# Kernel optimization log

Measured on AMD Instinct MI355X. Metric: run time of the kernel, lower is better.

The kernel has to match this reference:

```python
import jax, jax.numpy as jnp
import numpy as np

B, N, D = 256, 64, 256   # graphs, nodes/graph, hidden dim (node_size*extend_dim)
T, E = B * N, 524288     # total nodes, total edges
NODE, BOND, K = 128, 16, 3
RRELU_SLOPE = (1.0 / 8.0 + 1.0 / 3.0) / 2.0  # eval-mode RReLU slope


def rrelu(x):
    return jnp.where(x >= 0, x, RRELU_SLOPE * x)


def conv_step(x, src, dst, ea, Wn, We, bm, Ws, bs):
    # message on each edge, scatter-add to destination, self-transform + update
    msg = jax.nn.relu(x[src] @ Wn + ea @ We + bm)          # [E, D]
    agg = jax.ops.segment_sum(msg, dst, num_segments=T)    # [T, D]
    return jax.nn.relu(x @ Ws + agg + bs)


def readout(x):
    # GlobalPool: cat([mean, sum, sort_pool(k=3)], -1) -> [B, 5D]
    xr = x.reshape(B, N, D)
    mean, s = xr.mean(1), xr.sum(1)
    order = jnp.argsort(-xr[..., -1], axis=1)[:, :K]                      # [B, K]
    topk = jnp.take_along_axis(xr, order[..., None], axis=1).reshape(B, K * D)
    return jnp.concatenate([mean, s, topk], -1)


def dot_pool(x1, x2):
    # per-graph cross-molecule dot product, max & mean -> [B, 2]
    item = jnp.einsum('bnd,bmd->bnm', x1.reshape(B, N, D), x2.reshape(B, N, D))
    return jnp.stack([item.max((1, 2)), item.mean((1, 2))], -1)


def setup_inputs() -> dict:
    key = jax.random.key(0)
    ks = jax.random.split(key, 32)
    batch = jnp.repeat(jnp.arange(B, dtype=jnp.int64), N)
    off = jnp.repeat(jnp.arange(B, dtype=jnp.int64) * N, E // B)

    def edges(k):
        s = jax.random.randint(k, (2, E), 0, N).astype(jnp.int64) + off[None, :]
        return s

    def w(k, shape):
        fan = shape[0]
        return jax.random.normal(k, shape, jnp.float32) * (1.0 / np.sqrt(fan))

    return {
        'x1': jax.random.normal(ks[0], (T, NODE), jnp.float32),
        'edge_index1': edges(ks[1]),
        'edge_attr1': jax.random.normal(ks[2], (E, BOND), jnp.float32),
        'batch1': batch,
        'x2': jax.random.normal(ks[3], (T, NODE), jnp.float32),
        'edge_index2': edges(ks[4]),
        'edge_attr2': jax.random.normal(ks[5], (E, BOND), jnp.float32),
        'batch2': batch,
        'W0_1': w(ks[6], (NODE, D)), 'b0_1': jnp.zeros(D),
        'W0_2': w(ks[7], (NODE, D)), 'b0_2': jnp.zeros(D),
        'Wn1': w(ks[8], (D, D)), 'We1': w(ks[9], (BOND, D)), 'bm1': jnp.zeros(D),
        'Ws1': w(ks[10], (D, D)), 'bs1': jnp.zeros(D),
        'Wn2': w(ks[11], (D, D)), 'We2': w(ks[12], (BOND, D)), 'bm2': jnp.zeros(D),
        'Ws2': w(ks[13], (D, D)), 'bs2': jnp.zeros(D),
        'Wf1': w(ks[14], (5 * D, D)), 'bf1': jnp.zeros(D),
        'Wf2': w(ks[15], (5 * D, D)), 'bf2': jnp.zeros(D),
        'Wo1': w(ks[16], (2 * D + 6, D)), 'bo1': jnp.zeros(D),
        'Wo2': w(ks[17], (D, 2)), 'bo2': jnp.zeros(2),
    }


def reference(x1, edge_index1, edge_attr1, batch1, x2, edge_index2, edge_attr2, batch2,
              W0_1, b0_1, W0_2, b0_2,
              Wn1, We1, bm1, Ws1, bs1,
              Wn2, We2, bm2, Ws2, bs2,
              Wf1, bf1, Wf2, bf2, Wo1, bo1, Wo2, bo2):
    xm1 = rrelu(x1 @ W0_1 + b0_1)
    xm2 = rrelu(x2 @ W0_2 + b0_2)
    s1, d1 = edge_index1[0], edge_index1[1]
    s2, d2 = edge_index2[0], edge_index2[1]
    fusion = []
    for _ in range(3):  # message_steps
        xm1 = conv_step(xm1, s1, d1, edge_attr1, Wn1, We1, bm1, Ws1, bs1)
        xm2 = conv_step(xm2, s2, d2, edge_attr2, Wn2, We2, bm2, Ws2, bs2)
        fusion.append(dot_pool(xm1, xm2))
    outm1 = readout(xm1) @ Wf1 + bf1
    outm2 = readout(xm2) @ Wf2 + bf2
    out = jnp.concatenate([outm1, outm2, jnp.concatenate(fusion, -1)], -1)
    out = out @ Wo1 + bo1
    return out @ Wo2 + bo2
```

## Files before the change

### kernel.cpp

```cpp
#include <hip/hip_runtime.h>
#include <hip/hip_fp16.h>

#define E_TOTAL 524288
#define RRELU_SLOPE 0.22916666666666666f
#define NKSPLIT 10

typedef float f32x4 __attribute__((ext_vector_type(4)));
typedef short short8_t __attribute__((ext_vector_type(8)));
typedef _Float16 half4_t __attribute__((ext_vector_type(4)));
typedef _Float16 h2v __attribute__((ext_vector_type(2)));

#define MFMA16F16 __builtin_amdgcn_mfma_f32_16x16x16f16

#if defined(__HIP_DEVICE_COMPILE__)
# if __has_builtin(__builtin_amdgcn_cvt_pkrtz)
#  define HAVE_PKRTZ 1
# endif
#endif

__device__ inline unsigned short f2bf(float x) {
  unsigned int u = __float_as_uint(x);
  u += 0x7FFFu + ((u >> 16) & 1u);
  return (unsigned short)(u >> 16);
}

__device__ inline unsigned int pack_h2(float a, float b) {
  __half2 h = __floats2half2_rn(a, b);
  return __builtin_bit_cast(unsigned int, h);
}

__device__ inline unsigned int pack_h2_fast(float a, float b) {
#ifdef HAVE_PKRTZ
  return __builtin_bit_cast(unsigned int, __builtin_amdgcn_cvt_pkrtz(a, b));
#else
  return pack_h2(a, b);
#endif
}

__global__ __launch_bounds__(256) void gemm_bf16_dual(
    const float* __restrict__ A1, const unsigned short* __restrict__ BT1,
    const float* __restrict__ bias1, float* __restrict__ C1,
    unsigned short* __restrict__ Ch1,
    const float* __restrict__ A2, const unsigned short* __restrict__ BT2,
    const float* __restrict__ bias2, float* __restrict__ C2,
    unsigned short* __restrict__ Ch2,
    int lda, int ldc, int K, int act)
{
  const float* A = blockIdx.z ? A2 : A1;
  const unsigned short* BT = blockIdx.z ? BT2 : BT1;
  const float* bias = blockIdx.z ? bias2 : bias1;
  float* C = blockIdx.z ? C2 : C1;
  unsigned short* Ch = blockIdx.z ? Ch2 : Ch1;

  __shared__ unsigned short As[128][32];
  __shared__ unsigned short Bs[128][32];
  const int tid = threadIdx.x;
  const int bm = blockIdx.x, bn = blockIdx.y;
  const int w = tid >> 6, l = tid & 63;
  const int wm = (w & 1) * 64, wn = (w >> 1) * 64;
  const int q = l >> 4, r = l & 15;

  f32x4 acc[4][4];
  for (int i = 0; i < 4; ++i)
    for (int j = 0; j < 4; ++j)
      acc[i][j] = (f32x4){0.f, 0.f, 0.f, 0.f};

  const int sm = tid >> 1;
  const int sk = (tid & 1) * 16;
  const float* ap = A + (size_t)(bm * 128 + sm) * lda + sk;
  const unsigned short* bp = BT + (size_t)(bn * 128 + sm) * K + sk;

  for (int k0 = 0; k0 < K; k0 += 32) {
    float4 f0 = *(const float4*)(ap + k0);
    float4 f1 = *(const float4*)(ap + k0 + 4);
    float4 f2 = *(const float4*)(ap + k0 + 8);
    float4 f3 = *(const float4*)(ap + k0 + 12);
    uint4 p0, p1;
    p0.x = (unsigned)f2bf(f0.x) | ((unsigned)f2bf(f0.y) << 16);
    p0.y = (unsigned)f2bf(f0.z) | ((unsigned)f2bf(f0.w) << 16);
    p0.z = (unsigned)f2bf(f1.x) | ((unsigned)f2bf(f1.y) << 16);
    p0.w = (unsigned)f2bf(f1.z) | ((unsigned)f2bf(f1.w) << 16);
    p1.x = (unsigned)f2bf(f2.x) | ((unsigned)f2bf(f2.y) << 16);
    p1.y = (unsigned)f2bf(f2.z) | ((unsigned)f2bf(f2.w) << 16);
    p1.z = (unsigned)f2bf(f3.x) | ((unsigned)f2bf(f3.y) << 16);
    p1.w = (unsigned)f2bf(f3.z) | ((unsigned)f2bf(f3.w) << 16);
    *(uint4*)&As[sm][sk] = p0;
    *(uint4*)&As[sm][sk + 8] = p1;
    uint4 b0 = *(const uint4*)(bp + k0);
    uint4 b1 = *(const uint4*)(bp + k0 + 8);
    *(uint4*)&Bs[sm][sk] = b0;
    *(uint4*)&Bs[sm][sk + 8] = b1;
    __syncthreads();

    short8_t af[4], bfr[4];
    for (int mt = 0; mt < 4; ++mt)
      af[mt] = *(const short8_t*)&As[wm + mt * 16 + r][q * 8];
    for (int nt = 0; nt < 4; ++nt)
      bfr[nt] = *(const short8_t*)&Bs[wn + nt * 16 + r][q * 8];
    for (int mt = 0; mt < 4; ++mt)
      for (int nt = 0; nt < 4; ++nt)
        acc[mt][nt] = __builtin_amdgcn_mfma_f32_16x16x32_bf16(
            af[mt], bfr[nt], acc[mt][nt], 0, 0, 0);
    __syncthreads();
  }

  for (int nt = 0; nt < 4; ++nt) {
    int gc = bn * 128 + wn + nt * 16 + r;
    float bv = bias ? bias[gc] : 0.f;
    for (int mt = 0; mt < 4; ++mt) {
      int gm = bm * 128 + wm + mt * 16 + q * 4;
      for (int rr = 0; rr < 4; ++rr) {
        float v = acc[mt][nt][rr] + bv;
        if (act == 2) v = (v >= 0.f) ? v : v * RRELU_SLOPE;
        if (Ch) Ch[(size_t)(gm + rr) * ldc + gc] = f2bf(v);
        else    C[(size_t)(gm + rr) * ldc + gc] = v;
      }
    }
  }
}

__global__ __launch_bounds__(256) void gemm_h_dual(
    const unsigned short* __restrict__ Ah1, const unsigned short* __restrict__ BT1,
    const float* __restrict__ bias1, unsigned int* __restrict__ yp1,
    float* __restrict__ y2o1,
    const unsigned short* __restrict__ Ah2, const unsigned short* __restrict__ BT2,
    const float* __restrict__ bias2, unsigned int* __restrict__ yp2,
    float* __restrict__ y2o2,
    int K)
{
  const unsigned short* A = blockIdx.z ? Ah2 : Ah1;
  const unsigned short* BT = blockIdx.z ? BT2 : BT1;
  const float* bias = blockIdx.z ? bias2 : bias1;
  unsigned int* yp = blockIdx.z ? yp2 : yp1;
  float* y2o = blockIdx.z ? y2o2 : y2o1;

  __shared__ unsigned short As[128][32];
  __shared__ unsigned short Bs[128][32];
  const int tid = threadIdx.x;
  const int bm = blockIdx.x, bn = blockIdx.y;
  const int w = tid >> 6, l = tid & 63;
  const int wm = (w & 1) * 64;
  const int q = l >> 4, r = l & 15;
  const bool packed = bn < 2;
  const int wn2 = (w >> 1) * 32;
  const int wn = (w >> 1) * 64;

  int colb[4];
#pragma unroll
  for (int nt = 0; nt < 4; ++nt)
    colb[nt] = packed ? (wn2 + (nt & 1) * 16 + (nt >> 1) * 64) : (wn + nt * 16);

  f32x4 acc[4][4];
  for (int i = 0; i < 4; ++i)
    for (int j = 0; j < 4; ++j)
      acc[i][j] = (f32x4){0.f, 0.f, 0.f, 0.f};

  const int gr = l >> 2;
  const int gk = (l & 3) * 8;
  const unsigned short* aw = A + (size_t)(bm * 128 + w * 32 + gr) * K + gk;
  const unsigned short* bw = BT + (size_t)(bn * 128 + w * 32 + gr) * K + gk;

  for (int k0 = 0; k0 < K; k0 += 32) {
    __builtin_amdgcn_global_load_lds(
        (const __attribute__((address_space(1))) unsigned int*)(aw + k0),
        (__attribute__((address_space(3))) unsigned int*)&As[w * 32][0], 16, 0, 0);
    __builtin_amdgcn_global_load_lds(
        (const __attribute__((address_space(1))) unsigned int*)(aw + (size_t)16 * K + k0),
        (__attribute__((address_space(3))) unsigned int*)&As[w * 32 + 16][0], 16, 0, 0);
    __builtin_amdgcn_global_load_lds(
        (const __attribute__((address_space(1))) unsigned int*)(bw + k0),
        (__attribute__((address_space(3))) unsigned int*)&Bs[w * 32][0], 16, 0, 0);
    __builtin_amdgcn_global_load_lds(
        (const __attribute__((address_space(1))) unsigned int*)(bw + (size_t)16 * K + k0),
        (__attribute__((address_space(3))) unsigned int*)&Bs[w * 32 + 16][0], 16, 0, 0);
    __syncthreads();

    short8_t af[4], bfr[4];
    for (int mt = 0; mt < 4; ++mt)
      af[mt] = *(const short8_t*)&As[wm + mt * 16 + r][q * 8];
    for (int nt = 0; nt < 4; ++nt)
      bfr[nt] = *(const short8_t*)&Bs[colb[nt] + r][q * 8];
    for (int mt = 0; mt < 4; ++mt)
      for (int nt = 0; nt < 4; ++nt)
        acc[mt][nt] = __builtin_amdgcn_mfma_f32_16x16x32_bf16(
            af[mt], bfr[nt], acc[mt][nt], 0, 0, 0);
    __syncthreads();
  }

  if (packed) {
    for (int nt2 = 0; nt2 < 2; ++nt2) {
      int j = wn2 + nt2 * 16 + r;
      float blo = bias[bn * 128 + j];
      float bhi = bias[bn * 128 + j + 64];
      for (int mt = 0; mt < 4; ++mt) {
        int gm = bm * 128 + wm + mt * 16 + q * 4;
        for (int rr = 0; rr < 4; ++rr) {
          float lo = acc[mt][nt2][rr] + blo;
          float hi = acc[mt][nt2 + 2][rr] + bhi;
          yp[(size_t)(gm + rr) * 128 + bn * 64 + j] = pack_h2_fast(lo, hi);
        }
      }
    }
  } else {
    for (int nt = 0; nt < 4; ++nt) {
      int col = (bn - 2) * 128 + wn + nt * 16 + r;
      float bv = bias[256 + col];
      for (int mt = 0; mt < 4; ++mt) {
        int gm = bm * 128 + wm + mt * 16 + q * 4;
        for (int rr = 0; rr < 4; ++rr)
          y2o[(size_t)(gm + rr) * 256 + col] = acc[mt][nt][rr] + bv;
      }
    }
  }
}

__global__ __launch_bounds__(256) void gemm_splitk_dual(
    const float* __restrict__ A1, const unsigned short* __restrict__ BT1,
    float* __restrict__ P1,
    const float* __restrict__ A2, const unsigned short* __restrict__ BT2,
    float* __restrict__ P2)
{
  const int mol = blockIdx.z & 1;
  const int kc = blockIdx.z >> 1;
  const float* A = mol ? A2 : A1;
  const unsigned short* BT = mol ? BT2 : BT1;
  float* P = mol ? P2 : P1;
  const int K = 1280;

  __shared__ unsigned short As[64][32];
  __shared__ unsigned short Bs[64][32];
  const int tid = threadIdx.x;
  const int m0 = blockIdx.x * 64, n0 = blockIdx.y * 64;
  const int w = tid >> 6, l = tid & 63;
  const int wm = (w & 1) * 32, wn = (w >> 1) * 32;
  const int q = l >> 4, r = l & 15;

  f32x4 acc[2][2];
  for (int i = 0; i < 2; ++i)
    for (int j = 0; j < 2; ++j)
      acc[i][j] = (f32x4){0.f, 0.f, 0.f, 0.f};

  const int sm = tid >> 2;
  const int sk = (tid & 3) * 8;
  const float* ap = A + (size_t)(m0 + sm) * K + kc * 128 + sk;
  const unsigned short* bp = BT + (size_t)(n0 + sm) * K + kc * 128 + sk;

  for (int k0 = 0; k0 < 128; k0 += 32) {
    float4 f0 = *(const float4*)(ap + k0);
    float4 f1 = *(const float4*)(ap + k0 + 4);
    uint4 p0;
    p0.x = (unsigned)f2bf(f0.x) | ((unsigned)f2bf(f0.y) << 16);
    p0.y = (unsigned)f2bf(f0.z) | ((unsigned)f2bf(f0.w) << 16);
    p0.z = (unsigned)f2bf(f1.x) | ((unsigned)f2bf(f1.y) << 16);
    p0.w = (unsigned)f2bf(f1.z) | ((unsigned)f2bf(f1.w) << 16);
    *(uint4*)&As[sm][sk] = p0;
    *(uint4*)&Bs[sm][sk] = *(const uint4*)(bp + k0);
    __syncthreads();

    short8_t af[2], bfr[2];
    for (int mt = 0; mt < 2; ++mt)
      af[mt] = *(const short8_t*)&As[wm + mt * 16 + r][q * 8];
    for (int nt = 0; nt < 2; ++nt)
      bfr[nt] = *(const short8_t*)&Bs[wn + nt * 16 + r][q * 8];
    for (int mt = 0; mt < 2; ++mt)
      for (int nt = 0; nt < 2; ++nt)
        acc[mt][nt] = __builtin_amdgcn_mfma_f32_16x16x32_bf16(
            af[mt], bfr[nt], acc[mt][nt], 0, 0, 0);
    __syncthreads();
  }

  for (int nt = 0; nt < 2; ++nt) {
    int gc = n0 + wn + nt * 16 + r;
    for (int mt = 0; mt < 2; ++mt) {
      int gm = m0 + wm + mt * 16 + q * 4;
      for (int rr = 0; rr < 4; ++rr)
        P[((size_t)kc * 256 + gm + rr) * 256 + gc] = acc[mt][nt][rr];
    }
  }
}

__global__ __launch_bounds__(256) void sort_edges_dual(
    const int* __restrict__ ei1, const int* __restrict__ ei2,
    int* __restrict__ meta1, int* __restrict__ meta2,
    int* __restrict__ perm1, int* __restrict__ perm2,
    int* __restrict__ starts1, int* __restrict__ starts2)
{
  const int mol = blockIdx.x >> 8;
  const int g = blockIdx.x & 255;
  const int* eidx = mol ? ei2 : ei1;
  int* meta = mol ? meta2 : meta1;
  int* perm = mol ? perm2 : perm1;
  int* starts = mol ? starts2 : starts1;

  __shared__ int cnt[4][64];
  __shared__ int startS[65];
  __shared__ int cur[64];
  const int t = threadIdx.x, w = t >> 6;
  cnt[w][t & 63] = 0;
  if (t < 64) cur[t] = 0;
  __syncthreads();
  for (int i = t; i < 2048; i += 256)
    atomicAdd(&cnt[w][eidx[E_TOTAL + g * 2048 + i] & 63], 1);
  __syncthreads();
  if (t == 0) {
    int acc = 0;
    for (int n = 0; n < 64; ++n) {
      startS[n] = acc;
      acc += cnt[0][n] + cnt[1][n] + cnt[2][n] + cnt[3][n];
    }
    startS[64] = acc;
  }
  __syncthreads();
  if (t < 65) starts[g * 65 + t] = startS[t];
  for (int i = t; i < 2048; i += 256) {
    int s = eidx[g * 2048 + i] & 63;
    int d = eidx[E_TOTAL + g * 2048 + i] & 63;
    int p = startS[d] + atomicAdd(&cur[d], 1);
    meta[g * 2048 + p] = s | (d << 8);
    perm[g * 2048 + p] = i;
  }
}

__global__ __launch_bounds__(256) void ea_gather_pack_dual(
    const float* __restrict__ ea1, const float* __restrict__ ea2,
    const int* __restrict__ perm1, const int* __restrict__ perm2,
    unsigned int* __restrict__ o1, unsigned int* __restrict__ o2)
{
  const int mol = blockIdx.x >> 11;
  const float* ea = mol ? ea2 : ea1;
  const int* perm = mol ? perm2 : perm1;
  unsigned int* out = mol ? o2 : o1;
  int p = (blockIdx.x & 2047) * 256 + threadIdx.x;
  int g = p >> 11;
  int i = perm[p];
  const float* s = ea + (size_t)(g * 2048 + i) * 16;
  float4 v0 = *(const float4*)(s);
  float4 v1 = *(const float4*)(s + 4);
  float4 v2 = *(const float4*)(s + 8);
  float4 v3 = *(const float4*)(s + 12);
  uint4 q0, q1;
  q0.x = pack_h2(v0.x, v0.y); q0.y = pack_h2(v0.z, v0.w);
  q0.z = pack_h2(v1.x, v1.y); q0.w = pack_h2(v1.z, v1.w);
  q1.x = pack_h2(v2.x, v2.y); q1.y = pack_h2(v2.z, v2.w);
  q1.z = pack_h2(v3.x, v3.y); q1.w = pack_h2(v3.z, v3.w);
  *(uint4*)(out + (size_t)p * 8) = q0;
  *(uint4*)(out + (size_t)p * 8 + 4) = q1;
}

template <bool WR32>
__device__ __forceinline__ void edge_conv_body(
    const unsigned int* __restrict__ ypA, const float* __restrict__ y2A,
    const int* __restrict__ meta1,
    const unsigned int* __restrict__ eas1, const unsigned int* __restrict__ wep1,
    const int* __restrict__ st1, float* __restrict__ xo1,
    unsigned short* __restrict__ xoh1,
    const unsigned int* __restrict__ ypB, const float* __restrict__ y2B,
    const int* __restrict__ meta2,
    const unsigned int* __restrict__ eas2, const unsigned int* __restrict__ wep2,
    const int* __restrict__ st2, float* __restrict__ xo2,
    unsigned short* __restrict__ xoh2)
{
  const unsigned int* yp; const float* y2; const int* meta;
  const unsigned int* eas; const unsigned int* wep; const int* st;
  float* xo; unsigned short* xoh;
  if (blockIdx.z == 0) { yp = ypA; y2 = y2A; meta = meta1; eas = eas1; wep = wep1; st = st1; xo = xo1; xoh = xoh1; }
  else                 { yp = ypB; y2 = y2B; meta = meta2; eas = eas2; wep = wep2; st = st2; xo = xo2; xoh = xoh2; }

  __shared__ unsigned int ypk[4160];
  const int g = blockIdx.x >> 1;
  const int dbase = (blockIdx.x & 1) * 128;
  const int hb = (blockIdx.x & 1);
  const int tid = threadIdx.x;
  const int l = tid & 63;
  const int w = tid >> 6;
  const int rh = l & 15;
  const int qh = l >> 4;
  const int rhw = w * 8 + rh;

  for (int i = tid; i < 4096; i += 512) {
    int n = i >> 6, j = i & 63;
    ypk[n * 65 + j] = yp[(size_t)(g * 64 + n) * 128 + hb * 64 + j];
  }

  uint2 bfr[8];
#pragma unroll
  for (int c = 0; c < 8; ++c) {
    int d = dbase + c * 16 + rh;
    bfr[c].x = wep[(2 * qh) * 256 + d];
    bfr[c].y = wep[(2 * qh + 1) * 256 + d];
  }

  __syncthreads();

  const int estart = st[g * 65 + w * 8];
  const int eend   = st[g * 65 + w * 8 + 8];

  f32x4 acc[8];
#pragma unroll
  for (int i = 0; i < 8; ++i) acc[i] = (f32x4){0.f, 0.f, 0.f, 0.f};

  int base = estart;
  uint2 af = {0u, 0u};
  int mv = -1;
  if (base < eend) {
    int lim = eend - base; if (lim > 16) lim = 16;
    af = *(const uint2*)(eas + ((size_t)g * 2048 + base + (rh < lim ? rh : lim - 1)) * 8 + 2 * qh);
    int m = meta[(size_t)g * 2048 + base + (l < lim ? l : lim - 1)];
    mv = (l < lim) ? m : -1;
  }

  while (base < eend) {
    int mp[4];
#pragma unroll
    for (int v = 0; v < 4; ++v)
      mp[v] = __builtin_amdgcn_ds_bpermute(qh * 16 + v * 4, mv);

    int nbase = base + 16;
    uint2 afn = af;
    int mvn = -1;
    if (nbase < eend) {
      int nlim = eend - nbase; if (nlim > 16) nlim = 16;
      afn = *(const uint2*)(eas + ((size_t)g * 2048 + nbase + (rh < nlim ? rh : nlim - 1)) * 8 + 2 * qh);
      int m2 = meta[(size_t)g * 2048 + nbase + (l < nlim ? l : nlim - 1)];
      mvn = (l < nlim) ? m2 : -1;
    }

    half4_t afh = __builtin_bit_cast(half4_t, af);
    f32x4 pa[4], pb[4];
#pragma unroll
    for (int cp = 0; cp < 4; ++cp) {
      f32x4 z = (f32x4){0.f, 0.f, 0.f, 0.f};
      pa[cp] = MFMA16F16(afh, __builtin_bit_cast(half4_t, bfr[cp]), z, 0, 0, 0);
      pb[cp] = MFMA16F16(afh, __builtin_bit_cast(half4_t, bfr[cp + 4]), z, 0, 0, 0);
    }

    unsigned int yv[4][4];
    unsigned int ind[4];
#pragma unroll
    for (int v = 0; v < 4; ++v) {
      int sv = mp[v] & 63;
      int dv = (mp[v] >> 8) & 255;
      const unsigned int* yb = ypk + sv * 65 + rh;
      yv[0][v] = yb[0];
      yv[1][v] = yb[16];
      yv[2][v] = yb[32];
      yv[3][v] = yb[48];
      ind[v] = (dv == rhw) ? 0x3C00u : 0u;
    }
    uint2 su;
    su.x = ind[0] | (ind[1] << 16);
    su.y = ind[2] | (ind[3] << 16);
    half4_t sfrag = __builtin_bit_cast(half4_t, su);

    const h2v hz = {(_Float16)0.0f, (_Float16)0.0f};
#pragma unroll
    for (int cp = 0; cp < 4; ++cp) {
      unsigned int t[4];
#pragma unroll
      for (int v = 0; v < 4; ++v) {
        h2v s = __builtin_bit_cast(h2v, pack_h2_fast(pa[cp][v], pb[cp][v]));
        s = s + __builtin_bit_cast(h2v, yv[cp][v]);
        s = __builtin_elementwise_max(s, hz);
        t[v] = __builtin_bit_cast(unsigned int, s);
      }
      uint2 blo, bhi;
      blo.x = __builtin_amdgcn_perm(t[1], t[0], 0x05040100u);
      blo.y = __builtin_amdgcn_perm(t[3], t[2], 0x05040100u);
      bhi.x = __builtin_amdgcn_perm(t[1], t[0], 0x07060302u);
      bhi.y = __builtin_amdgcn_perm(t[3], t[2], 0x07060302u);
      acc[cp]     = MFMA16F16(sfrag, __builtin_bit_cast(half4_t, blo), acc[cp], 0, 0, 0);
      acc[cp + 4] = MFMA16F16(sfrag, __builtin_bit_cast(half4_t, bhi), acc[cp + 4], 0, 0, 0);
    }

    base = nbase;
    af = afn;
    mv = mvn;
  }

  if (qh < 2) {
#pragma unroll
    for (int v = 0; v < 4; ++v) {
      int node = g * 64 + w * 8 + qh * 4 + v;
      const float* ysp = y2 + (size_t)node * 256 + dbase + rh;
      float* xop = xo + (size_t)node * 256 + dbase + rh;
      unsigned short* xohp = xoh + (size_t)node * 256 + dbase + rh;
#pragma unroll
      for (int cp = 0; cp < 8; ++cp) {
        int dim = (cp & 3) * 16 + (cp >> 2) * 64;
        float val = fmaxf(ysp[dim] + acc[cp][v], 0.f);
        if (WR32) xop[dim] = val;
        xohp[dim] = f2bf(val);
      }
    }
  }
}

__global__ __launch_bounds__(512, 4) void edge_conv_dual_wf(
    const unsigned int* __restrict__ ypA, const float* __restrict__ y2A,
    const int* __restrict__ meta1,
    const unsigned int* __restrict__ eas1, const unsigned int* __restrict__ wep1,
    const int* __restrict__ st1, float* __restrict__ xo1,
    unsigned short* __restrict__ xoh1,
    const unsigned int* __restrict__ ypB, const float* __restrict__ y2B,
    const int* __restrict__ meta2,
    const unsigned int* __restrict__ eas2, const unsigned int* __restrict__ wep2,
    const int* __restrict__ st2, float* __restrict__ xo2,
    unsigned short* __restrict__ xoh2)
{
  edge_conv_body<true>(ypA, y2A, meta1, eas1, wep1, st1, xo1, xoh1,
                       ypB, y2B, meta2, eas2, wep2, st2, xo2, xoh2);
}

__global__ __launch_bounds__(512, 4) void edge_conv_dual_nf(
    const unsigned int* __restrict__ ypA, const float* __restrict__ y2A,
    const int* __restrict__ meta1,
    const unsigned int* __restrict__ eas1, const unsigned int* __restrict__ wep1,
    const int* __restrict__ st1, float* __restrict__ xo1,
    unsigned short* __restrict__ xoh1,
    const unsigned int* __restrict__ ypB, const float* __restrict__ y2B,
    const int* __restrict__ meta2,
    const unsigned int* __restrict__ eas2, const unsigned int* __restrict__ wep2,
    const int* __restrict__ st2, float* __restrict__ xo2,
    unsigned short* __restrict__ xoh2)
{
  edge_conv_body<false>(ypA, y2A, meta1, eas1, wep1, st1, xo1, xoh1,
                        ypB, y2B, meta2, eas2, wep2, st2, xo2, xoh2);
}

__global__ __launch_bounds__(256) void dot_pool_mfma(
    const unsigned short* __restrict__ x1h, const unsigned short* __restrict__ x2h,
    float* __restrict__ fusion, int step)
{
  __shared__ unsigned short s1[64][256];
  __shared__ unsigned short s2[64][256];
  const int g = blockIdx.x, tid = threadIdx.x;
  const int l = tid & 63, w = tid >> 6;
  const int r = l & 15, q = l >> 4;

  for (int i = tid; i < 2048; i += 256) {
    int row = i >> 5, c = i & 31;
    int cs = c ^ (row & 7);
    *(uint4*)&s1[row][cs * 8] = *(const uint4*)(x1h + (size_t)(g * 64 + row) * 256 + c * 8);
    *(uint4*)&s2[row][cs * 8] = *(const uint4*)(x2h + (size_t)(g * 64 + row) * 256 + c * 8);
  }
  __syncthreads();

  const int m0 = w * 16;
  const int sx = r & 7;
  f32x4 acc[4];
#pragma unroll
  for (int nt = 0; nt < 4; ++nt) acc[nt] = (f32x4){0.f, 0.f, 0.f, 0.f};

#pragma unroll
  for (int kb = 0; kb < 32; kb += 4) {
    int ch = (kb + q) ^ sx;
    short8_t af = *(const short8_t*)&s1[m0 + r][ch * 8];
#pragma unroll
    for (int nt = 0; nt < 4; ++nt) {
      short8_t bf = *(const short8_t*)&s2[nt * 16 + r][ch * 8];
      acc[nt] = __builtin_amdgcn_mfma_f32_16x16x32_bf16(af, bf, acc[nt], 0, 0, 0);
    }
  }

  float mymax = -1e30f, mysum = 0.f;
#pragma unroll
  for (int nt = 0; nt < 4; ++nt)
#pragma unroll
    for (int reg = 0; reg < 4; ++reg) {
      float v = acc[nt][reg];
      mymax = fmaxf(mymax, v);
      mysum += v;
    }
  for (int off = 32; off; off >>= 1) {
    mymax = fmaxf(mymax, __shfl_down(mymax, off, 64));
    mysum += __shfl_down(mysum, off, 64);
  }
  __syncthreads();
  float* red = (float*)&s1[0][0];
  if (l == 0) { red[w] = mymax; red[8 + w] = mysum; }
  __syncthreads();
  if (tid == 0) {
    float gm = fmaxf(fmaxf(red[0], red[1]), fmaxf(red[2], red[3]));
    float gs = red[8] + red[9] + red[10] + red[11];
    fusion[g * 6 + step * 2] = gm;
    fusion[g * 6 + step * 2 + 1] = gs * (1.f / 4096.f);
  }
}

__global__ __launch_bounds__(256) void readout_dual(
    const float* __restrict__ xm1, const float* __restrict__ xm2,
    float* __restrict__ R1, float* __restrict__ R2)
{
  const int mol = blockIdx.x >> 8;
  const float* xm = mol ? xm2 : xm1;
  float* R = mol ? R2 : R1;
  __shared__ float lastcol[64];
  __shared__ int topi[3];
  const int g = blockIdx.x & 255, d = threadIdx.x;
  float s = 0.f;
  for (int n = 0; n < 64; ++n) s += xm[(size_t)(g * 64 + n) * 256 + d];
  R[(size_t)g * 1280 + d] = s * (1.f / 64.f);
  R[(size_t)g * 1280 + 256 + d] = s;
  if (d < 64) lastcol[d] = xm[(size_t)(g * 64 + d) * 256 + 255];
  __syncthreads();
  if (d == 0) {
    unsigned long long used = 0;
    for (int j = 0; j < 3; ++j) {
      float best = -1e30f;
      int bi = 0;
      for (int n = 0; n < 64; ++n) {
        if ((used >> n) & 1ull) continue;
        if (lastcol[n] > best) { best = lastcol[n]; bi = n; }
      }
      used |= (1ull << bi);
      topi[j] = bi;
    }
  }
  __syncthreads();
  for (int j = 0; j < 3; ++j)
    R[(size_t)g * 1280 + 512 + j * 256 + d] =
        xm[(size_t)(g * 64 + topi[j]) * 256 + d];
}

__global__ __launch_bounds__(256) void final_head(
    const float* __restrict__ P1, const float* __restrict__ P2,
    const float* __restrict__ bf1, const float* __restrict__ bf2,
    const float* __restrict__ fusion,
    const float* __restrict__ Wo1, const float* __restrict__ bo1,
    const float* __restrict__ Wo2, const float* __restrict__ bo2,
    float* __restrict__ out)
{
  __shared__ float cat[520];
  __shared__ float r0s[4], r1s[4];
  const int g = blockIdx.x, t = threadIdx.x;
  float s1 = bf1[t], s2 = bf2[t];
#pragma unroll
  for (int k = 0; k < NKSPLIT; ++k) {
    s1 += P1[((size_t)k * 256 + g) * 256 + t];
    s2 += P2[((size_t)k * 256 + g) * 256 + t];
  }
  cat[t] = s1;
  cat[256 + t] = s2;
  if (t < 6) cat[512 + t] = fusion[g * 6 + t];
  __syncthreads();
  float a0 = 0.f, a1 = 0.f, a2 = 0.f, a3 = 0.f;
  for (int k = 0; k < 516; k += 4) {
    a0 = fmaf(cat[k],     Wo1[(size_t)(k)     * 256 + t], a0);
    a1 = fmaf(cat[k + 1], Wo1[(size_t)(k + 1) * 256 + t], a1);
    a2 = fmaf(cat[k + 2], Wo1[(size_t)(k + 2) * 256 + t], a2);
    a3 = fmaf(cat[k + 3], Wo1[(size_t)(k + 3) * 256 + t], a3);
  }
  a0 = fmaf(cat[516], Wo1[(size_t)516 * 256 + t], a0);
  a1 = fmaf(cat[517], Wo1[(size_t)517 * 256 + t], a1);
  float acc = bo1[t] + ((a0 + a1) + (a2 + a3));
  float p0 = acc * Wo2[t * 2];
  float p1 = acc * Wo2[t * 2 + 1];
  for (int off = 32; off; off >>= 1) {
    p0 += __shfl_down(p0, off, 64);
    p1 += __shfl_down(p1, off, 64);
  }
  if ((t & 63) == 0) { r0s[t >> 6] = p0; r1s[t >> 6] = p1; }
  __syncthreads();
  if (t == 0) {
    out[g * 2] = r0s[0] + r0s[1] + r0s[2] + r0s[3] + bo2[0];
    out[g * 2 + 1] = r1s[0] + r1s[1] + r1s[2] + r1s[3] + bo2[1];
  }
}

__global__ __launch_bounds__(256) void transpose_all(
    const float* __restrict__ W0_1, const float* __restrict__ W0_2,
    const float* __restrict__ Wn1, const float* __restrict__ Ws1,
    const float* __restrict__ Wn2, const float* __restrict__ Ws2,
    const float* __restrict__ Wf1, const float* __restrict__ Wf2,
    unsigned short* __restrict__ W0T1, unsigned short* __restrict__ W0T2,
    unsigned short* __restrict__ WcT1, unsigned short* __restrict__ WcT2,
    unsigned short* __restrict__ WfT1, unsigned short* __restrict__ WfT2)
{
  const int b = blockIdx.x;
  const float* src; unsigned short* dst; int k0, K;
  if (b < 2)       { src = W0_1; dst = W0T1;         K = 128;  k0 = b * 64; }
  else if (b < 4)  { src = W0_2; dst = W0T2;         K = 128;  k0 = (b - 2) * 64; }
  else if (b < 8)  { src = Wn1;  dst = WcT1;         K = 256;  k0 = (b - 4) * 64; }
  else if (b < 12) { src = Ws1;  dst = WcT1 + 65536; K = 256;  k0 = (b - 8) * 64; }
  else if (b < 16) { src = Wn2;  dst = WcT2;         K = 256;  k0 = (b - 12) * 64; }
  else if (b < 20) { src = Ws2;  dst = WcT2 + 65536; K = 256;  k0 = (b - 16) * 64; }
  else if (b < 40) { src = Wf1;  dst = WfT1;         K = 1280; k0 = (b - 20) * 64; }
  else             { src = Wf2;  dst = WfT2;         K = 1280; k0 = (b - 40) * 64; }

  __shared__ unsigned short t[64][258];
  const int tid = threadIdx.x;
  for (int i = tid; i < 16384; i += 256) {
    int row = i >> 8, col = i & 255;
    t[row][col] = f2bf(src[(size_t)(k0 + row) * 256 + col]);
  }
  __syncthreads();
  unsigned short* dp = dst + (size_t)tid * K + k0;
  for (int k = 0; k < 64; k += 8) {
    uint4 v;
    v.x = (unsigned)t[k + 0][tid] | ((unsigned)t[k + 1][tid] << 16);
    v.y = (unsigned)t[k + 2][tid] | ((unsigned)t[k + 3][tid] << 16);
    v.z = (unsigned)t[k + 4][tid] | ((unsigned)t[k + 5][tid] << 16);
    v.w = (unsigned)t[k + 6][tid] | ((unsigned)t[k + 7][tid] << 16);
    *(uint4*)(dp + k) = v;
  }
}

__global__ void misc_prep(
    const float* bm1, const float* bs1, const float* bm2, const float* bs2,
    const float* We1, const float* We2,
    float* bcat1, float* bcat2,
    unsigned int* weh1, unsigned int* weh2)
{
  int idx = blockIdx.x * 256 + threadIdx.x;
  if (idx < 512) {
    bcat1[idx] = idx < 256 ? bm1[idx] : bs1[idx - 256];
  } else if (idx < 1024) {
    int i = idx - 512;
    bcat2[i] = i < 256 ? bm2[i] : bs2[i - 256];
  } else if (idx < 3072) {
    int i = idx - 1024, j = i >> 8, d = i & 255;
    weh1[i] = pack_h2(We1[(2 * j) * 256 + d], We1[(2 * j + 1) * 256 + d]);
  } else if (idx < 5120) {
    int i = idx - 3072, j = i >> 8, d = i & 255;
    weh2[i] = pack_h2(We2[(2 * j) * 256 + d], We2[(2 * j + 1) * 256 + d]);
  }
}

extern "C" void kernel_launch(void* const* d_in, const int* in_sizes, int n_in,
                              void* d_out, int out_size, void* d_ws, size_t ws_size,
                              hipStream_t stream)
{
  const float* x1 = (const float*)d_in[0];
  const int* ei1 = (const int*)d_in[1];
  const float* ea1 = (const float*)d_in[2];
  const float* x2 = (const float*)d_in[4];
  const int* ei2 = (const int*)d_in[5];
  const float* ea2 = (const float*)d_in[6];
  const float* W0_1 = (const float*)d_in[8];
  const float* b0_1 = (const float*)d_in[9];
  const float* W0_2 = (const float*)d_in[10];
  const float* b0_2 = (const float*)d_in[11];
  const float* Wn1 = (const float*)d_in[12];
  const float* We1 = (const float*)d_in[13];
  const float* bm1 = (const float*)d_in[14];
  const float* Ws1 = (const float*)d_in[15];
  const float* bs1 = (const float*)d_in[16];
  const float* Wn2 = (const float*)d_in[17];
  const float* We2 = (const float*)d_in[18];
  const float* bm2 = (const float*)d_in[19];
  const float* Ws2 = (const float*)d_in[20];
  const float* bs2 = (const float*)d_in[21];
  const float* Wf1 = (const float*)d_in[22];
  const float* bf1 = (const float*)d_in[23];
  const float* Wf2 = (const float*)d_in[24];
  const float* bf2 = (const float*)d_in[25];
  const float* Wo1 = (const float*)d_in[26];
  const float* bo1 = (const float*)d_in[27];
  const float* Wo2 = (const float*)d_in[28];
  const float* bo2 = (const float*)d_in[29];
  float* out = (float*)d_out;

  float* w = (float*)d_ws;
  size_t off = 0;
  auto alloc = [&](size_t nf) { float* p = w + off; off += nf; return p; };
  float* xmA1 = alloc(4194304);
  float* xmA2 = alloc(4194304);
  float* xmB1 = alloc(4194304);
  float* xmB2 = alloc(4194304);
  unsigned int* yp1 = (unsigned int*)alloc(2097152);
  unsigned int* yp2 = (unsigned int*)alloc(2097152);
  float* y2a1 = alloc(4194304);
  float* y2a2 = alloc(4194304);
  float* R1 = alloc(327680);
  float* R2 = alloc(327680);
  float* P1 = alloc(655360);
  float* P2 = alloc(655360);
  float* fusion = alloc(1536);
  float* bcat1 = alloc(512);
  float* bcat2 = alloc(512);
  unsigned short* W0T1 = (unsigned short*)alloc(16384);
  unsigned short* W0T2 = (unsigned short*)alloc(16384);
  unsigned short* WcT1 = (unsigned short*)alloc(65536);
  unsigned short* WcT2 = (unsigned short*)alloc(65536);
  unsigned short* WfT1 = (unsigned short*)alloc(163840);
  unsigned short* WfT2 = (unsigned short*)alloc(163840);
  unsigned int* weh1 = (unsigned int*)alloc(2048);
  unsigned int* weh2 = (unsigned int*)alloc(2048);
  unsigned int* eah1 = (unsigned int*)alloc(4194304);
  unsigned int* eah2 = (unsigned int*)alloc(4194304);
  int* meta1 = (int*)alloc(524288);
  int* meta2 = (int*)alloc(524288);
  int* perm1 = (int*)alloc(524288);
  int* perm2 = (int*)alloc(524288);
  int* starts1 = (int*)alloc(16640);
  int* starts2 = (int*)alloc(16640);
  unsigned short* xmhA1 = (unsigned short*)alloc(2097152);
  unsigned short* xmhA2 = (unsigned short*)alloc(2097152);
  unsigned short* xmhB1 = (unsigned short*)alloc(2097152);
  unsigned short* xmhB2 = (unsigned short*)alloc(2097152);
  (void)in_sizes; (void)n_in; (void)out_size; (void)ws_size;

  sort_edges_dual<<<512, 256, 0, stream>>>(ei1, ei2, meta1, meta2,
                                           perm1, perm2, starts1, starts2);
  transpose_all<<<60, 256, 0, stream>>>(W0_1, W0_2, Wn1, Ws1, Wn2, Ws2,
                                        Wf1, Wf2, W0T1, W0T2, WcT1, WcT2,
                                        WfT1, WfT2);
  misc_prep<<<20, 256, 0, stream>>>(bm1, bs1, bm2, bs2, We1, We2,
                                    bcat1, bcat2, weh1, weh2);
  ea_gather_pack_dual<<<4096, 256, 0, stream>>>(ea1, ea2, perm1, perm2,
                                                eah1, eah2);

  gemm_bf16_dual<<<dim3(128, 2, 2), 256, 0, stream>>>(
      x1, W0T1, b0_1, nullptr, xmhA1, x2, W0T2, b0_2, nullptr, xmhA2,
      128, 256, 128, 2);

  float* cur1 = xmA1; float* cur2 = xmA2;
  float* nxt1 = xmB1; float* nxt2 = xmB2;
  unsigned short* curh1 = xmhA1; unsigned short* curh2 = xmhA2;
  unsigned short* nxth1 = xmhB1; unsigned short* nxth2 = xmhB2;
  for (int step = 0; step < 3; ++step) {
    gemm_h_dual<<<dim3(128, 4, 2), 256, 0, stream>>>(
        curh1, WcT1, bcat1, yp1, y2a1, curh2, WcT2, bcat2, yp2, y2a2, 256);
    if (step == 2) {
      edge_conv_dual_wf<<<dim3(512, 1, 2), 512, 0, stream>>>(
          yp1, y2a1, meta1, eah1, weh1, starts1, nxt1, nxth1,
          yp2, y2a2, meta2, eah2, weh2, starts2, nxt2, nxth2);
    } else {
      edge_conv_dual_nf<<<dim3(512, 1, 2), 512, 0, stream>>>(
          yp1, y2a1, meta1, eah1, weh1, starts1, nxt1, nxth1,
          yp2, y2a2, meta2, eah2, weh2, starts2, nxt2, nxth2);
    }
    dot_pool_mfma<<<256, 256, 0, stream>>>(nxth1, nxth2, fusion, step);
    float* t1 = cur1; cur1 = nxt1; nxt1 = t1;
    float* t2 = cur2; cur2 = nxt2; nxt2 = t2;
    unsigned short* th1 = curh1; curh1 = nxth1; nxth1 = th1;
    unsigned short* th2 = curh2; curh2 = nxth2; nxth2 = th2;
  }

  readout_dual<<<512, 256, 0, stream>>>(cur1, cur2, R1, R2);
  gemm_splitk_dual<<<dim3(4, 4, 2 * NKSPLIT), 256, 0, stream>>>(
      R1, WfT1, P1, R2, WfT2, P2);
  final_head<<<256, 256, 0, stream>>>(P1, P2, bf1, bf2, fusion,
                                      Wo1, bo1, Wo2, bo2, out);
}
```

Baseline: 477.9 us.

## Process full hidden dim per edge-conv block to reuse edge metadata

Each edge-conv block now covers one whole graph across both 128-wide halves of the hidden dimension instead of one half, so the grid shrinks from 512 to 256 blocks per molecule. Edge attributes, metadata loads, bpermutes and the scatter indicator fragment are computed once per edge tile and reused for both halves. The cost is twice the shared memory, more registers for the doubled accumulators and B fragments, and half as many blocks, which lowers occupancy and parallelism on the GPU.

```diff
diff --git a/kernel.cpp b/kernel.cpp
--- a/kernel.cpp
+++ b/kernel.cpp
@@ -366,10 +366,8 @@
   if (blockIdx.z == 0) { yp = ypA; y2 = y2A; meta = meta1; eas = eas1; wep = wep1; st = st1; xo = xo1; xoh = xoh1; }
   else                 { yp = ypB; y2 = y2B; meta = meta2; eas = eas2; wep = wep2; st = st2; xo = xo2; xoh = xoh2; }
 
-  __shared__ unsigned int ypk[4160];
-  const int g = blockIdx.x >> 1;
-  const int dbase = (blockIdx.x & 1) * 128;
-  const int hb = (blockIdx.x & 1);
+  __shared__ unsigned int ypk[8320];
+  const int g = blockIdx.x;
   const int tid = threadIdx.x;
   const int l = tid & 63;
   const int w = tid >> 6;
@@ -377,27 +375,31 @@
   const int qh = l >> 4;
   const int rhw = w * 8 + rh;
 
-  for (int i = tid; i < 4096; i += 512) {
-    int n = i >> 6, j = i & 63;
-    ypk[n * 65 + j] = yp[(size_t)(g * 64 + n) * 128 + hb * 64 + j];
-  }
-
-  uint2 bfr[8];
-#pragma unroll
-  for (int c = 0; c < 8; ++c) {
-    int d = dbase + c * 16 + rh;
-    bfr[c].x = wep[(2 * qh) * 256 + d];
-    bfr[c].y = wep[(2 * qh + 1) * 256 + d];
-  }
+  for (int i = tid; i < 8192; i += 512) {
+    int hb = i >> 12, n = (i >> 6) & 63, j = i & 63;
+    ypk[hb * 4160 + n * 65 + j] = yp[(size_t)(g * 64 + n) * 128 + hb * 64 + j];
+  }
+
+  uint2 bfr[2][8];
+#pragma unroll
+  for (int hb = 0; hb < 2; ++hb)
+#pragma unroll
+    for (int c = 0; c < 8; ++c) {
+      int d = hb * 128 + c * 16 + rh;
+      bfr[hb][c].x = wep[(2 * qh) * 256 + d];
+      bfr[hb][c].y = wep[(2 * qh + 1) * 256 + d];
+    }
 
   __syncthreads();
 
   const int estart = st[g * 65 + w * 8];
   const int eend   = st[g * 65 + w * 8 + 8];
 
-  f32x4 acc[8];
-#pragma unroll
-  for (int i = 0; i < 8; ++i) acc[i] = (f32x4){0.f, 0.f, 0.f, 0.f};
+  f32x4 acc[2][8];
+#pragma unroll
+  for (int hb = 0; hb < 2; ++hb)
+#pragma unroll
+    for (int i = 0; i < 8; ++i) acc[hb][i] = (f32x4){0.f, 0.f, 0.f, 0.f};
 
   int base = estart;
   uint2 af = {0u, 0u};
@@ -425,51 +427,59 @@
       mvn = (l < nlim) ? m2 : -1;
     }
 
-    half4_t afh = __builtin_bit_cast(half4_t, af);
-    f32x4 pa[4], pb[4];
-#pragma unroll
-    for (int cp = 0; cp < 4; ++cp) {
-      f32x4 z = (f32x4){0.f, 0.f, 0.f, 0.f};
-      pa[cp] = MFMA16F16(afh, __builtin_bit_cast(half4_t, bfr[cp]), z, 0, 0, 0);
-      pb[cp] = MFMA16F16(afh, __builtin_bit_cast(half4_t, bfr[cp + 4]), z, 0, 0, 0);
-    }
-
-    unsigned int yv[4][4];
+    int sv[4];
     unsigned int ind[4];
 #pragma unroll
     for (int v = 0; v < 4; ++v) {
-      int sv = mp[v] & 63;
+      sv[v] = mp[v] & 63;
       int dv = (mp[v] >> 8) & 255;
-      const unsigned int* yb = ypk + sv * 65 + rh;
-      yv[0][v] = yb[0];
-      yv[1][v] = yb[16];
-      yv[2][v] = yb[32];
-      yv[3][v] = yb[48];
       ind[v] = (dv == rhw) ? 0x3C00u : 0u;
     }
     uint2 su;
     su.x = ind[0] | (ind[1] << 16);
     su.y = ind[2] | (ind[3] << 16);
     half4_t sfrag = __builtin_bit_cast(half4_t, su);
+    half4_t afh = __builtin_bit_cast(half4_t, af);
 
     const h2v hz = {(_Float16)0.0f, (_Float16)0.0f};
 #pragma unroll
-    for (int cp = 0; cp < 4; ++cp) {
-      unsigned int t[4];
+    for (int hb = 0; hb < 2; ++hb) {
+      f32x4 pa[4], pb[4];
+#pragma unroll
+      for (int cp = 0; cp < 4; ++cp) {
+        f32x4 z = (f32x4){0.f, 0.f, 0.f, 0.f};
+        pa[cp] = MFMA16F16(afh, __builtin_bit_cast(half4_t, bfr[hb][cp]), z, 0, 0, 0);
+        pb[cp] = MFMA16F16(afh, __builtin_bit_cast(half4_t, bfr[hb][cp + 4]), z, 0, 0, 0);
+      }
+
+      unsigned int yv[4][4];
 #pragma unroll
       for (int v = 0; v < 4; ++v) {
-        h2v s = __builtin_bit_cast(h2v, pack_h2_fast(pa[cp][v], pb[cp][v]));
-        s = s + __builtin_bit_cast(h2v, yv[cp][v]);
-        s = __builtin_elementwise_max(s, hz);
-        t[v] = __builtin_bit_cast(unsigned int, s);
+        const unsigned int* yb = ypk + hb * 4160 + sv[v] * 65 + rh;
+        yv[0][v] = yb[0];
+        yv[1][v] = yb[16];
+        yv[2][v] = yb[32];
+        yv[3][v] = yb[48];
       }
-      uint2 blo, bhi;
-      blo.x = __builtin_amdgcn_perm(t[1], t[0], 0x05040100u);
-      blo.y = __builtin_amdgcn_perm(t[3], t[2], 0x05040100u);
-      bhi.x = __builtin_amdgcn_perm(t[1], t[0], 0x07060302u);
-      bhi.y = __builtin_amdgcn_perm(t[3], t[2], 0x07060302u);
-      acc[cp]     = MFMA16F16(sfrag, __builtin_bit_cast(half4_t, blo), acc[cp], 0, 0, 0);
-      acc[cp + 4] = MFMA16F16(sfrag, __builtin_bit_cast(half4_t, bhi), acc[cp + 4], 0, 0, 0);
+
+#pragma unroll
+      for (int cp = 0; cp < 4; ++cp) {
+        unsigned int t[4];
+#pragma unroll
+        for (int v = 0; v < 4; ++v) {
+          h2v s = __builtin_bit_cast(h2v, pack_h2_fast(pa[cp][v], pb[cp][v]));
+          s = s + __builtin_bit_cast(h2v, yv[cp][v]);
+          s = __builtin_elementwise_max(s, hz);
+          t[v] = __builtin_bit_cast(unsigned int, s);
+        }
+        uint2 blo, bhi;
+        blo.x = __builtin_amdgcn_perm(t[1], t[0], 0x05040100u);
+        blo.y = __builtin_amdgcn_perm(t[3], t[2], 0x05040100u);
+        bhi.x = __builtin_amdgcn_perm(t[1], t[0], 0x07060302u);
+        bhi.y = __builtin_amdgcn_perm(t[3], t[2], 0x07060302u);
+        acc[hb][cp]     = MFMA16F16(sfrag, __builtin_bit_cast(half4_t, blo), acc[hb][cp], 0, 0, 0);
+        acc[hb][cp + 4] = MFMA16F16(sfrag, __builtin_bit_cast(half4_t, bhi), acc[hb][cp + 4], 0, 0, 0);
+      }
     }
 
     base = nbase;
@@ -481,16 +491,18 @@
 #pragma unroll
     for (int v = 0; v < 4; ++v) {
       int node = g * 64 + w * 8 + qh * 4 + v;
-      const float* ysp = y2 + (size_t)node * 256 + dbase + rh;
-      float* xop = xo + (size_t)node * 256 + dbase + rh;
-      unsigned short* xohp = xoh + (size_t)node * 256 + dbase + rh;
-#pragma unroll
-      for (int cp = 0; cp < 8; ++cp) {
-        int dim = (cp & 3) * 16 + (cp >> 2) * 64;
-        float val = fmaxf(ysp[dim] + acc[cp][v], 0.f);
-        if (WR32) xop[dim] = val;
-        xohp[dim] = f2bf(val);
-      }
+      const float* ysp = y2 + (size_t)node * 256 + rh;
+      float* xop = xo + (size_t)node * 256 + rh;
+      unsigned short* xohp = xoh + (size_t)node * 256 + rh;
+#pragma unroll
+      for (int hb = 0; hb < 2; ++hb)
+#pragma unroll
+        for (int cp = 0; cp < 8; ++cp) {
+          int dim = hb * 128 + (cp & 3) * 16 + (cp >> 2) * 64;
+          float val = fmaxf(ysp[dim] + acc[hb][cp][v], 0.f);
+          if (WR32) xop[dim] = val;
+          xohp[dim] = f2bf(val);
+        }
     }
   }
 }
@@ -822,11 +834,11 @@
     gemm_h_dual<<<dim3(128, 4, 2), 256, 0, stream>>>(
         curh1, WcT1, bcat1, yp1, y2a1, curh2, WcT2, bcat2, yp2, y2a2, 256);
     if (step == 2) {
-      edge_conv_dual_wf<<<dim3(512, 1, 2), 512, 0, stream>>>(
+      edge_conv_dual_wf<<<dim3(256, 1, 2), 512, 0, stream>>>(
           yp1, y2a1, meta1, eah1, weh1, starts1, nxt1, nxth1,
           yp2, y2a2, meta2, eah2, weh2, starts2, nxt2, nxth2);
     } else {
-      edge_conv_dual_nf<<<dim3(512, 1, 2), 512, 0, stream>>>(
+      edge_conv_dual_nf<<<dim3(256, 1, 2), 512, 0, stream>>>(
           yp1, y2a1, meta1, eah1, weh1, starts1, nxt1, nxth1,
           yp2, y2a2, meta2, eah2, weh2, starts2, nxt2, nxth2);
     }
```

New measurement: 536.9 us. +12.4%, slower.
